# Kernel tuning notes

Measured on AMD Instinct MI355X. Metric: run time of the kernel, lower is better.

## Reference

```python
import jax, jax.numpy as jnp
import numpy as np

DIM = 768
HEADS = 8
DHEAD = 64
DEMB = HEADS * DHEAD  # 512
EPS = 1e-5


def layer_norm(x, g, b):
    mu = jnp.mean(x, axis=-1, keepdims=True)
    var = jnp.var(x, axis=-1, keepdims=True)
    return (x - mu) * jax.lax.rsqrt(var + EPS) * g + b


def setup_inputs() -> dict:
    key = jax.random.key(0)
    ks = jax.random.split(key, 9)
    b, t, n_src, n_ltn = 2, 4, 8192, 64
    inv = 1.0 / np.sqrt(DIM)
    return {
        "src": jax.random.normal(ks[0], (b, t, n_src, DIM), jnp.float32),
        "ltn": jax.random.normal(ks[1], (b, t, n_ltn, DIM), jnp.float32),
        "g_src": jnp.ones((DIM,), jnp.float32),
        "b_src": jnp.zeros((DIM,), jnp.float32),
        "g_ltn": jnp.ones((DIM,), jnp.float32),
        "b_ltn": jnp.zeros((DIM,), jnp.float32),
        # weights stored (in, out) so y = x @ W  (== torch Linear with W.T)
        "Wq": jax.random.normal(ks[2], (DIM, DEMB), jnp.float32) * inv,
        "Wkv": jax.random.normal(ks[3], (DIM, 2 * DEMB), jnp.float32) * inv,
        "Wo": jax.random.normal(ks[4], (DEMB, DIM), jnp.float32) * (1.0 / np.sqrt(DEMB)),
    }


def reference(src, ltn, g_src, b_src, g_ltn, b_ltn, Wq, Wkv, Wo):
    b, t, n_ltn, _ = ltn.shape
    n_src = src.shape[2]
    scale = DHEAD ** -0.5

    src_n = layer_norm(src, g_src, b_src)
    ltn_n = layer_norm(ltn, g_ltn, b_ltn)

    q = ltn_n @ Wq                                  # [b,t,nl,DEMB]
    ctx = jnp.concatenate([src_n, ltn_n], axis=-2)  # [b,t,ns+nl,DIM]
    kv = ctx @ Wkv                                  # [b,t,ns+nl,2*DEMB]
    k, v = jnp.split(kv, 2, axis=-1)

    def to_heads(x):  # b t n (h d) -> b h t n d
        B, T, N, _ = x.shape
        return x.reshape(B, T, N, HEADS, DHEAD).transpose(0, 3, 1, 2, 4)

    q, k, v = to_heads(q), to_heads(k), to_heads(v)

    attn = jnp.einsum('bhtid,bhtjd->bhtij', q, k) * scale
    attn = jax.nn.softmax(attn - jax.lax.stop_gradient(attn.max(axis=-1, keepdims=True)), axis=-1)
    out = jnp.einsum('bhtij,bhtjd->bhtid', attn, v)  # [b,h,t,nl,d]

    out = out.transpose(0, 2, 3, 1, 4).reshape(b, t, n_ltn, DEMB)
    return out @ Wo
```

## Files before the change

kernel.cpp:

```cpp
#include <hip/hip_runtime.h>
#include <hip/hip_bf16.h>
#include <type_traits>


#define N_SRC 8192
#define N_LTN 64
#define N_CTX 8256
#define NBT 8
#define MROWS 66048
#define DIMK 768
#define DEMB 512
#define NSPLIT 32
#define NTILES 65

typedef short short8 __attribute__((ext_vector_type(8)));
typedef float floatx4 __attribute__((ext_vector_type(4)));
typedef __attribute__((address_space(1))) void gvoid;
typedef __attribute__((address_space(3))) void lvoid;

__device__ inline ushort f2bf(float f) {
    union { float f; unsigned u; } v; v.f = f;
    unsigned u = v.u;
    return (ushort)((u + 0x7fffu + ((u >> 16) & 1u)) >> 16);
}

__global__ __launch_bounds__(256) void transpose_all(
        const float* __restrict__ Wkv, const float* __restrict__ Wq,
        const float* __restrict__ Wo, ushort* __restrict__ WkvT,
        ushort* __restrict__ WqT, ushort* __restrict__ WoT) {
    __shared__ ushort tile[64][65];
    int z = blockIdx.z;
    const float* in; ushort* out; int R, C;
    if (z == 0)      { in = Wkv; out = WkvT; R = 768; C = 1024; }
    else if (z == 1) { in = Wq;  out = WqT;  R = 768; C = 512;  }
    else             { in = Wo;  out = WoT;  R = 512; C = 768;  }
    int C0 = blockIdx.x * 64, R0 = blockIdx.y * 64;
    if (C0 >= C || R0 >= R) return;
    int tc = threadIdx.x & 63, tr4 = threadIdx.x >> 6;
#pragma unroll
    for (int j = 0; j < 16; j++) {
        int r = tr4 + j * 4;
        tile[r][tc] = f2bf(in[(size_t)(R0 + r) * C + C0 + tc]);
    }
    __syncthreads();
#pragma unroll
    for (int j = 0; j < 16; j++) {
        int c = tr4 + j * 4;
        out[(size_t)(C0 + c) * R + R0 + tc] = tile[tc][c];
    }
}

__global__ __launch_bounds__(256) void ln_kernel(
        const float* __restrict__ src, const float* __restrict__ ltn,
        const float* __restrict__ gs, const float* __restrict__ bs,
        const float* __restrict__ gl, const float* __restrict__ bl,
        ushort* __restrict__ ctx, ushort* __restrict__ qin) {
    int r = blockIdx.x * 4 + (threadIdx.x >> 6);
    int lane = threadIdx.x & 63;
    int bt = r / N_CTX;
    int i = r - bt * N_CTX;
    const float *x, *g, *b;
    int isl = (i >= N_SRC);
    if (!isl) { x = src + ((size_t)bt * N_SRC + i) * DIMK; g = gs; b = bs; }
    else      { x = ltn + ((size_t)bt * N_LTN + (i - N_SRC)) * DIMK; g = gl; b = bl; }
    float4 v[3]; float s = 0.f, s2 = 0.f;
#pragma unroll
    for (int t = 0; t < 3; t++) {
        float4 xv = *(const float4*)(x + t * 256 + lane * 4);
        v[t] = xv;
        s  += xv.x + xv.y + xv.z + xv.w;
        s2 += xv.x * xv.x + xv.y * xv.y + xv.z * xv.z + xv.w * xv.w;
    }
#pragma unroll
    for (int off = 32; off >= 1; off >>= 1) {
        s  += __shfl_xor(s,  off, 64);
        s2 += __shfl_xor(s2, off, 64);
    }
    float mu  = s * (1.0f / 768.0f);
    float var = s2 * (1.0f / 768.0f) - mu * mu;
    float rs  = rsqrtf(var + 1e-5f);
    ushort* crow = ctx + (size_t)r * DIMK;
    ushort* qrow = isl ? (qin + (size_t)(bt * N_LTN + (i - N_SRC)) * DIMK) : nullptr;
#pragma unroll
    for (int t = 0; t < 3; t++) {
        int idx = t * 256 + lane * 4;
        float4 gv = *(const float4*)(g + idx);
        float4 bv = *(const float4*)(b + idx);
        ushort4 u;
        u.x = f2bf((v[t].x - mu) * rs * gv.x + bv.x);
        u.y = f2bf((v[t].y - mu) * rs * gv.y + bv.y);
        u.z = f2bf((v[t].z - mu) * rs * gv.z + bv.z);
        u.w = f2bf((v[t].w - mu) * rs * gv.w + bv.w);
        *(ushort4*)(crow + idx) = u;
        if (isl) *(ushort4*)(qrow + idx) = u;
    }
}

template <typename CT>
__global__ __launch_bounds__(256) void gemm_bt(
        const ushort* __restrict__ A, const ushort* __restrict__ B,
        CT* __restrict__ C, int M, int N, int K) {
    __shared__ ushort lA[128 * 64];
    __shared__ ushort lB[128 * 64];
    int tid = threadIdx.x;
    int lane = tid & 63, wave = tid >> 6;
    int wm = wave >> 1, wn = wave & 1;
    int bn = blockIdx.x, bm = blockIdx.y;

    floatx4 acc[4][4];
#pragma unroll
    for (int mi = 0; mi < 4; mi++)
#pragma unroll
        for (int ni = 0; ni < 4; ni++) acc[mi][ni] = (floatx4){0.f, 0.f, 0.f, 0.f};

    int srow = lane >> 3;
    int schunk = (lane & 7) ^ srow;
    int quad = lane >> 4, lr = lane & 15;
    const int kiters = K >> 6;

    for (int kt = 0; kt < kiters; kt++) {
#pragma unroll
        for (int c2 = 0; c2 < 4; c2++) {
            int row = c2 * 32 + wave * 8 + srow;
            const ushort* gpA = A + ((size_t)(bm * 128 + row) * K + kt * 64 + schunk * 8);
            ushort* lpA = lA + (c2 * 32 + wave * 8) * 64 + lane * 8;
            __builtin_amdgcn_global_load_lds((gvoid*)gpA, (lvoid*)lpA, 16, 0, 0);
            const ushort* gpB = B + ((size_t)(bn * 128 + row) * K + kt * 64 + schunk * 8);
            ushort* lpB = lB + (c2 * 32 + wave * 8) * 64 + lane * 8;
            __builtin_amdgcn_global_load_lds((gvoid*)gpB, (lvoid*)lpB, 16, 0, 0);
        }
        __syncthreads();
#pragma unroll
        for (int ks = 0; ks < 2; ks++) {
            short8 av[4], bv[4];
            int slot = ((ks * 4 + quad) ^ (lane & 7)) * 8;
#pragma unroll
            for (int mi = 0; mi < 4; mi++)
                av[mi] = *(const short8*)(lA + (wm * 64 + mi * 16 + lr) * 64 + slot);
#pragma unroll
            for (int ni = 0; ni < 4; ni++)
                bv[ni] = *(const short8*)(lB + (wn * 64 + ni * 16 + lr) * 64 + slot);
#pragma unroll
            for (int mi = 0; mi < 4; mi++)
#pragma unroll
                for (int ni = 0; ni < 4; ni++)
                    acc[mi][ni] = __builtin_amdgcn_mfma_f32_16x16x32_bf16(
                        av[mi], bv[ni], acc[mi][ni], 0, 0, 0);
        }
        __syncthreads();
    }
#pragma unroll
    for (int mi = 0; mi < 4; mi++)
#pragma unroll
        for (int ni = 0; ni < 4; ni++)
#pragma unroll
            for (int r = 0; r < 4; r++) {
                int row = bm * 128 + wm * 64 + mi * 16 + quad * 4 + r;
                int col = bn * 128 + wn * 64 + ni * 16 + lr;
                float vv = acc[mi][ni][r];
                if constexpr (std::is_same<CT, ushort>::value)
                    C[(size_t)row * N + col] = f2bf(vv);
                else
                    C[(size_t)row * N + col] = vv;
            }
}

#define PR 136

__global__ __launch_bounds__(256) void attn_flash(
        const float* __restrict__ qf, const ushort* __restrict__ kvb,
        float* __restrict__ Op, float* __restrict__ ml) {
    __shared__ ushort lK[128 * 64];
    __shared__ ushort lVT[64 * PR];
    __shared__ ushort lP[64 * PR];
    __shared__ float smax[64 * 4];
    __shared__ float psum[64 * 4];
    __shared__ float mnew[64];
    __shared__ float salpha[64];

    int comb = blockIdx.x, split = blockIdx.y;
    int bt = comb >> 3, h = comb & 7;
    int tid = threadIdx.x;
    int w = tid >> 6, lane = tid & 63, quad = lane >> 4, lr = lane & 15;

    const ushort* kptr = kvb + (size_t)bt * N_CTX * 1024 + h * 64;
    const ushort* vptr = kptr + 512;

    short8 qa[4][2];
    {
        const float* qbase = qf + (size_t)(bt * 64) * DEMB + h * 64;
#pragma unroll
        for (int mi = 0; mi < 4; mi++)
#pragma unroll
            for (int kc = 0; kc < 2; kc++) {
                const float* p = qbase + (size_t)(mi * 16 + lr) * DEMB + kc * 32 + quad * 8;
                float4 f0 = *(const float4*)p;
                float4 f1 = *(const float4*)(p + 4);
                short8 v;
                v[0] = f2bf(f0.x); v[1] = f2bf(f0.y); v[2] = f2bf(f0.z); v[3] = f2bf(f0.w);
                v[4] = f2bf(f1.x); v[5] = f2bf(f1.y); v[6] = f2bf(f1.z); v[7] = f2bf(f1.w);
                qa[mi][kc] = v;
            }
    }

    floatx4 accO[4];
#pragma unroll
    for (int nt = 0; nt < 4; nt++) accO[nt] = (floatx4){0.f, 0.f, 0.f, 0.f};
    float m_run = -1e30f, l_run = 0.f;

    int vp = tid & 63;
    int vdg = tid >> 6;

    for (int t = split; t < NTILES; t += NSPLIT) {
        int kbase = t * 128;
        __syncthreads();

#pragma unroll
        for (int c2 = 0; c2 < 4; c2++) {
            int jloc = w * 32 + c2 * 8 + (lane >> 3);
            int chunk = (lane & 7) ^ ((lane >> 3) & 7);
            int jg = kbase + jloc; if (jg > N_CTX - 1) jg = N_CTX - 1;
            const ushort* gp = kptr + (size_t)jg * 1024 + chunk * 8;
            ushort* lp = lK + (w * 32 + c2 * 8) * 64 + lane * 8;
            __builtin_amdgcn_global_load_lds((gvoid*)gp, (lvoid*)lp, 16, 0, 0);
        }

        {
            int k0 = kbase + vp * 2;
            bool valid = (k0 + 1) < N_CTX;
            int k0c = valid ? k0 : (N_CTX - 2);
            const ushort* r0 = vptr + (size_t)k0c * 1024 + vdg * 16;
            const ushort* r1 = r0 + 1024;
            uint4 a0 = *(const uint4*)r0;
            uint4 a1 = *(const uint4*)(r0 + 8);
            uint4 b0 = *(const uint4*)r1;
            uint4 b1 = *(const uint4*)(r1 + 8);
            if (!valid) {
                a0 = make_uint4(0, 0, 0, 0); a1 = a0; b0 = a0; b1 = a0;
            }
            unsigned av8[8] = {a0.x, a0.y, a0.z, a0.w, a1.x, a1.y, a1.z, a1.w};
            unsigned bv8[8] = {b0.x, b0.y, b0.z, b0.w, b1.x, b1.y, b1.z, b1.w};
#pragma unroll
            for (int i = 0; i < 8; i++) {
                unsigned la = av8[i] & 0xffffu, ha = av8[i] >> 16;
                unsigned lb = bv8[i] & 0xffffu, hb = bv8[i] >> 16;
                *(unsigned*)(lVT + (vdg * 16 + 2 * i) * PR + vp * 2)     = la | (lb << 16);
                *(unsigned*)(lVT + (vdg * 16 + 2 * i + 1) * PR + vp * 2) = ha | (hb << 16);
            }
        }
        __syncthreads();

        floatx4 accS[4][2];
#pragma unroll
        for (int mi = 0; mi < 4; mi++)
#pragma unroll
            for (int nt = 0; nt < 2; nt++) accS[mi][nt] = (floatx4){0.f, 0.f, 0.f, 0.f};
#pragma unroll
        for (int kc = 0; kc < 2; kc++) {
            short8 bv[2];
#pragma unroll
            for (int nt = 0; nt < 2; nt++) {
                int kr = w * 32 + nt * 16 + lr;
                int slot = (kc * 4 + quad) ^ (kr & 7);
                bv[nt] = *(const short8*)(lK + kr * 64 + slot * 8);
            }
#pragma unroll
            for (int mi = 0; mi < 4; mi++)
#pragma unroll
                for (int nt = 0; nt < 2; nt++)
                    accS[mi][nt] = __builtin_amdgcn_mfma_f32_16x16x32_bf16(
                        qa[mi][kc], bv[nt], accS[mi][nt], 0, 0, 0);
        }

        bool v0 = (kbase + w * 32 + lr) < N_CTX;
        bool v1 = (kbase + w * 32 + 16 + lr) < N_CTX;
        float sc[4][2][4];
#pragma unroll
        for (int mi = 0; mi < 4; mi++)
#pragma unroll
            for (int r = 0; r < 4; r++) {
                sc[mi][0][r] = v0 ? accS[mi][0][r] * 0.125f : -1e30f;
                sc[mi][1][r] = v1 ? accS[mi][1][r] * 0.125f : -1e30f;
            }
#pragma unroll
        for (int mi = 0; mi < 4; mi++)
#pragma unroll
            for (int r = 0; r < 4; r++) {
                float m = fmaxf(sc[mi][0][r], sc[mi][1][r]);
#pragma unroll
                for (int d = 1; d < 16; d <<= 1) m = fmaxf(m, __shfl_xor(m, d, 64));
                if (lr == 0) smax[(mi * 16 + quad * 4 + r) * 4 + w] = m;
            }
        __syncthreads();

        if (w == 0) {
            float4 s4 = *(const float4*)(smax + lane * 4);
            float mt = fmaxf(fmaxf(s4.x, s4.y), fmaxf(s4.z, s4.w));
            float mn = fmaxf(m_run, mt);
            salpha[lane] = __expf(m_run - mn);
            m_run = mn;
            mnew[lane] = mn;
        }
        __syncthreads();

#pragma unroll
        for (int mi = 0; mi < 4; mi++)
#pragma unroll
            for (int r = 0; r < 4; r++) {
                int row = mi * 16 + quad * 4 + r;
                float mrow = mnew[row];
                float p0 = __expf(sc[mi][0][r] - mrow);
                float p1 = __expf(sc[mi][1][r] - mrow);
                lP[row * PR + w * 32 + lr]      = f2bf(p0);
                lP[row * PR + w * 32 + 16 + lr] = f2bf(p1);
                float s = p0 + p1;
#pragma unroll
                for (int d = 1; d < 16; d <<= 1) s += __shfl_xor(s, d, 64);
                if (lr == 0) psum[row * 4 + w] = s;
            }
        {
            float a0 = salpha[w * 16 + quad * 4 + 0];
            float a1 = salpha[w * 16 + quad * 4 + 1];
            float a2 = salpha[w * 16 + quad * 4 + 2];
            float a3 = salpha[w * 16 + quad * 4 + 3];
#pragma unroll
            for (int nt = 0; nt < 4; nt++) {
                accO[nt][0] *= a0; accO[nt][1] *= a1;
                accO[nt][2] *= a2; accO[nt][3] *= a3;
            }
        }
        __syncthreads();

        if (w == 0) {
            float4 p4 = *(const float4*)(psum + lane * 4);
            l_run = l_run * salpha[lane] + (p4.x + p4.y + p4.z + p4.w);
        }

        short8 av[4];
#pragma unroll
        for (int kc = 0; kc < 4; kc++)
            av[kc] = *(const short8*)(lP + (w * 16 + lr) * PR + kc * 32 + quad * 8);
#pragma unroll
        for (int nt = 0; nt < 4; nt++)
#pragma unroll
            for (int kc = 0; kc < 4; kc++) {
                short8 bv = *(const short8*)(lVT + (nt * 16 + lr) * PR + kc * 32 + quad * 8);
                accO[nt] = __builtin_amdgcn_mfma_f32_16x16x32_bf16(av[kc], bv, accO[nt], 0, 0, 0);
            }
    }

    float* opb = Op + (size_t)(comb * NSPLIT + split) * 64 * 64;
#pragma unroll
    for (int nt = 0; nt < 4; nt++)
#pragma unroll
        for (int r = 0; r < 4; r++)
            opb[(w * 16 + quad * 4 + r) * 64 + nt * 16 + lr] = accO[nt][r];
    if (w == 0) {
        float* mlp = ml + ((size_t)(comb * NSPLIT + split) * 64 + lane) * 2;
        mlp[0] = m_run; mlp[1] = l_run;
    }
}

__global__ __launch_bounds__(64) void attn_combine(
        const float* __restrict__ Op, const float* __restrict__ ml,
        ushort* __restrict__ outp) {
    int bx = blockIdx.x;
    int comb = bx >> 6, q = bx & 63;
    int bt = comb >> 3, h = comb & 7;
    int d = threadIdx.x;
    float M = -1e30f;
    for (int s = 0; s < NSPLIT; s++)
        M = fmaxf(M, ml[((size_t)(comb * NSPLIT + s) * 64 + q) * 2]);
    float L = 0.f, O = 0.f;
    for (int s = 0; s < NSPLIT; s++) {
        const float* p = ml + ((size_t)(comb * NSPLIT + s) * 64 + q) * 2;
        float wgt = __expf(p[0] - M);
        L = fmaf(wgt, p[1], L);
        O = fmaf(wgt, Op[((size_t)(comb * NSPLIT + s) * 64 + q) * 64 + d], O);
    }
    outp[(size_t)(bt * 64 + q) * DEMB + h * 64 + d] = f2bf(O / L);
}

extern "C" void kernel_launch(void* const* d_in, const int* in_sizes, int n_in,
                              void* d_out, int out_size, void* d_ws, size_t ws_size,
                              hipStream_t stream) {
    const float* src   = (const float*)d_in[0];
    const float* ltn   = (const float*)d_in[1];
    const float* g_src = (const float*)d_in[2];
    const float* b_src = (const float*)d_in[3];
    const float* g_ltn = (const float*)d_in[4];
    const float* b_ltn = (const float*)d_in[5];
    const float* Wq    = (const float*)d_in[6];
    const float* Wkv   = (const float*)d_in[7];
    const float* Wo    = (const float*)d_in[8];
    float* out = (float*)d_out;

    char* ws = (char*)d_ws;
    size_t off = 0;
    auto alloc = [&](size_t bytes) -> void* {
        void* p = ws + off;
        off += (bytes + 255) & ~(size_t)255;
        return p;
    };
    ushort* ctx  = (ushort*)alloc((size_t)MROWS * DIMK * 2);
    ushort* qin  = (ushort*)alloc((size_t)512 * DIMK * 2);
    ushort* WkvT = (ushort*)alloc((size_t)1024 * DIMK * 2);
    ushort* WqT  = (ushort*)alloc((size_t)512 * DIMK * 2);
    ushort* WoT  = (ushort*)alloc((size_t)768 * DEMB * 2);
    ushort* kvb  = (ushort*)alloc((size_t)MROWS * 1024 * 2);
    float*  qf   = (float*) alloc((size_t)512 * DEMB * 4);
    ushort* outp = (ushort*)alloc((size_t)512 * DEMB * 2);

    float* Op  = (float*)(void*)ctx;
    float* mlb = Op + (size_t)64 * NSPLIT * 64 * 64;

    transpose_all<<<dim3(16, 12, 3), 256, 0, stream>>>(Wkv, Wq, Wo, WkvT, WqT, WoT);

    ln_kernel<<<MROWS / 4, 256, 0, stream>>>(src, ltn, g_src, b_src, g_ltn, b_ltn, ctx, qin);

    gemm_bt<ushort><<<dim3(1024 / 128, MROWS / 128), 256, 0, stream>>>(
        ctx, WkvT, kvb, MROWS, 1024, DIMK);
    gemm_bt<float><<<dim3(512 / 128, 512 / 128), 256, 0, stream>>>(
        qin, WqT, qf, 512, 512, DIMK);

    attn_flash<<<dim3(64, NSPLIT), 256, 0, stream>>>(qf, kvb, Op, mlb);
    attn_combine<<<4096, 64, 0, stream>>>(Op, mlb, outp);

    gemm_bt<float><<<dim3(768 / 128, 512 / 128), 256, 0, stream>>>(
        outp, WoT, out, 512, 768, DEMB);
}
```

Baseline: 568.5 us.

## Give each wave its own query rows in flash attention and halve the split count

Restructures the attention kernel so that each wave owns 16 query rows across all 128 keys of a tile, not 32 keys across all 64 rows. Row max and row sum now come from in-wave shuffles, which removes the shared-memory reduction arrays and two block barriers per tile. The number of KV splits drops from 32 to 16, so each block handles more tiles, the grid shrinks, and the combine step reads fewer partials. In exchange, each wave holds more score registers and reads all 128 K rows from LDS, and the smaller grid may leave compute units underused.

```diff
diff --git a/kernel.cpp b/kernel.cpp
--- a/kernel.cpp
+++ b/kernel.cpp
@@ -10,7 +10,7 @@
 #define MROWS 66048
 #define DIMK 768
 #define DEMB 512
-#define NSPLIT 32
+#define NSPLIT 16
 #define NTILES 65
 
 typedef short short8 __attribute__((ext_vector_type(8)));
@@ -173,10 +173,6 @@
     __shared__ ushort lK[128 * 64];
     __shared__ ushort lVT[64 * PR];
     __shared__ ushort lP[64 * PR];
-    __shared__ float smax[64 * 4];
-    __shared__ float psum[64 * 4];
-    __shared__ float mnew[64];
-    __shared__ float salpha[64];
 
     int comb = blockIdx.x, split = blockIdx.y;
     int bt = comb >> 3, h = comb & 7;
@@ -186,30 +182,27 @@
     const ushort* kptr = kvb + (size_t)bt * N_CTX * 1024 + h * 64;
     const ushort* vptr = kptr + 512;
 
-    short8 qa[4][2];
+    short8 qa[2];
     {
-        const float* qbase = qf + (size_t)(bt * 64) * DEMB + h * 64;
-#pragma unroll
-        for (int mi = 0; mi < 4; mi++)
-#pragma unroll
-            for (int kc = 0; kc < 2; kc++) {
-                const float* p = qbase + (size_t)(mi * 16 + lr) * DEMB + kc * 32 + quad * 8;
-                float4 f0 = *(const float4*)p;
-                float4 f1 = *(const float4*)(p + 4);
-                short8 v;
-                v[0] = f2bf(f0.x); v[1] = f2bf(f0.y); v[2] = f2bf(f0.z); v[3] = f2bf(f0.w);
-                v[4] = f2bf(f1.x); v[5] = f2bf(f1.y); v[6] = f2bf(f1.z); v[7] = f2bf(f1.w);
-                qa[mi][kc] = v;
-            }
+        const float* p0 = qf + (size_t)(bt * 64 + w * 16 + lr) * DEMB + h * 64;
+#pragma unroll
+        for (int kc = 0; kc < 2; kc++) {
+            const float* p = p0 + kc * 32 + quad * 8;
+            float4 f0 = *(const float4*)p;
+            float4 f1 = *(const float4*)(p + 4);
+            short8 v;
+            v[0] = f2bf(f0.x); v[1] = f2bf(f0.y); v[2] = f2bf(f0.z); v[3] = f2bf(f0.w);
+            v[4] = f2bf(f1.x); v[5] = f2bf(f1.y); v[6] = f2bf(f1.z); v[7] = f2bf(f1.w);
+            qa[kc] = v;
+        }
     }
 
     floatx4 accO[4];
 #pragma unroll
     for (int nt = 0; nt < 4; nt++) accO[nt] = (floatx4){0.f, 0.f, 0.f, 0.f};
-    float m_run = -1e30f, l_run = 0.f;
-
-    int vp = tid & 63;
-    int vdg = tid >> 6;
+    float m_run[4], l_run[4];
+#pragma unroll
+    for (int r = 0; r < 4; r++) { m_run[r] = -1e30f; l_run[r] = 0.f; }
 
     for (int t = split; t < NTILES; t += NSPLIT) {
         int kbase = t * 128;
@@ -226,10 +219,10 @@
         }
 
         {
-            int k0 = kbase + vp * 2;
+            int k0 = kbase + lane * 2;
             bool valid = (k0 + 1) < N_CTX;
             int k0c = valid ? k0 : (N_CTX - 2);
-            const ushort* r0 = vptr + (size_t)k0c * 1024 + vdg * 16;
+            const ushort* r0 = vptr + (size_t)k0c * 1024 + w * 16;
             const ushort* r1 = r0 + 1024;
             uint4 a0 = *(const uint4*)r0;
             uint4 a1 = *(const uint4*)(r0 + 8);
@@ -244,96 +237,72 @@
             for (int i = 0; i < 8; i++) {
                 unsigned la = av8[i] & 0xffffu, ha = av8[i] >> 16;
                 unsigned lb = bv8[i] & 0xffffu, hb = bv8[i] >> 16;
-                *(unsigned*)(lVT + (vdg * 16 + 2 * i) * PR + vp * 2)     = la | (lb << 16);
-                *(unsigned*)(lVT + (vdg * 16 + 2 * i + 1) * PR + vp * 2) = ha | (hb << 16);
+                *(unsigned*)(lVT + (w * 16 + 2 * i) * PR + lane * 2)     = la | (lb << 16);
+                *(unsigned*)(lVT + (w * 16 + 2 * i + 1) * PR + lane * 2) = ha | (hb << 16);
             }
         }
         __syncthreads();
 
-        floatx4 accS[4][2];
-#pragma unroll
-        for (int mi = 0; mi < 4; mi++)
-#pragma unroll
-            for (int nt = 0; nt < 2; nt++) accS[mi][nt] = (floatx4){0.f, 0.f, 0.f, 0.f};
+        floatx4 accS[8];
+#pragma unroll
+        for (int nt = 0; nt < 8; nt++) accS[nt] = (floatx4){0.f, 0.f, 0.f, 0.f};
 #pragma unroll
         for (int kc = 0; kc < 2; kc++) {
-            short8 bv[2];
-#pragma unroll
-            for (int nt = 0; nt < 2; nt++) {
-                int kr = w * 32 + nt * 16 + lr;
+#pragma unroll
+            for (int nt = 0; nt < 8; nt++) {
+                int kr = nt * 16 + lr;
                 int slot = (kc * 4 + quad) ^ (kr & 7);
-                bv[nt] = *(const short8*)(lK + kr * 64 + slot * 8);
-            }
-#pragma unroll
-            for (int mi = 0; mi < 4; mi++)
-#pragma unroll
-                for (int nt = 0; nt < 2; nt++)
-                    accS[mi][nt] = __builtin_amdgcn_mfma_f32_16x16x32_bf16(
-                        qa[mi][kc], bv[nt], accS[mi][nt], 0, 0, 0);
-        }
-
-        bool v0 = (kbase + w * 32 + lr) < N_CTX;
-        bool v1 = (kbase + w * 32 + 16 + lr) < N_CTX;
-        float sc[4][2][4];
-#pragma unroll
-        for (int mi = 0; mi < 4; mi++)
+                short8 bv = *(const short8*)(lK + kr * 64 + slot * 8);
+                accS[nt] = __builtin_amdgcn_mfma_f32_16x16x32_bf16(
+                    qa[kc], bv, accS[nt], 0, 0, 0);
+            }
+        }
+
+        float sc[8][4];
+        float tmax[4] = {-1e30f, -1e30f, -1e30f, -1e30f};
+#pragma unroll
+        for (int nt = 0; nt < 8; nt++) {
+            bool vk = (kbase + nt * 16 + lr) < N_CTX;
 #pragma unroll
             for (int r = 0; r < 4; r++) {
-                sc[mi][0][r] = v0 ? accS[mi][0][r] * 0.125f : -1e30f;
-                sc[mi][1][r] = v1 ? accS[mi][1][r] * 0.125f : -1e30f;
-            }
-#pragma unroll
-        for (int mi = 0; mi < 4; mi++)
+                float s = vk ? accS[nt][r] * 0.125f : -1e30f;
+                sc[nt][r] = s;
+                tmax[r] = fmaxf(tmax[r], s);
+            }
+        }
+#pragma unroll
+        for (int r = 0; r < 4; r++) {
+#pragma unroll
+            for (int d = 1; d < 16; d <<= 1) tmax[r] = fmaxf(tmax[r], __shfl_xor(tmax[r], d, 64));
+        }
+        float alpha[4], lsum[4];
+#pragma unroll
+        for (int r = 0; r < 4; r++) {
+            float mn = fmaxf(m_run[r], tmax[r]);
+            alpha[r] = __expf(m_run[r] - mn);
+            m_run[r] = mn;
+            lsum[r] = 0.f;
+        }
+
+#pragma unroll
+        for (int nt = 0; nt < 8; nt++) {
 #pragma unroll
             for (int r = 0; r < 4; r++) {
-                float m = fmaxf(sc[mi][0][r], sc[mi][1][r]);
-#pragma unroll
-                for (int d = 1; d < 16; d <<= 1) m = fmaxf(m, __shfl_xor(m, d, 64));
-                if (lr == 0) smax[(mi * 16 + quad * 4 + r) * 4 + w] = m;
-            }
-        __syncthreads();
-
-        if (w == 0) {
-            float4 s4 = *(const float4*)(smax + lane * 4);
-            float mt = fmaxf(fmaxf(s4.x, s4.y), fmaxf(s4.z, s4.w));
-            float mn = fmaxf(m_run, mt);
-            salpha[lane] = __expf(m_run - mn);
-            m_run = mn;
-            mnew[lane] = mn;
-        }
-        __syncthreads();
-
-#pragma unroll
-        for (int mi = 0; mi < 4; mi++)
-#pragma unroll
-            for (int r = 0; r < 4; r++) {
-                int row = mi * 16 + quad * 4 + r;
-                float mrow = mnew[row];
-                float p0 = __expf(sc[mi][0][r] - mrow);
-                float p1 = __expf(sc[mi][1][r] - mrow);
-                lP[row * PR + w * 32 + lr]      = f2bf(p0);
-                lP[row * PR + w * 32 + 16 + lr] = f2bf(p1);
-                float s = p0 + p1;
-#pragma unroll
-                for (int d = 1; d < 16; d <<= 1) s += __shfl_xor(s, d, 64);
-                if (lr == 0) psum[row * 4 + w] = s;
-            }
-        {
-            float a0 = salpha[w * 16 + quad * 4 + 0];
-            float a1 = salpha[w * 16 + quad * 4 + 1];
-            float a2 = salpha[w * 16 + quad * 4 + 2];
-            float a3 = salpha[w * 16 + quad * 4 + 3];
-#pragma unroll
-            for (int nt = 0; nt < 4; nt++) {
-                accO[nt][0] *= a0; accO[nt][1] *= a1;
-                accO[nt][2] *= a2; accO[nt][3] *= a3;
-            }
-        }
-        __syncthreads();
-
-        if (w == 0) {
-            float4 p4 = *(const float4*)(psum + lane * 4);
-            l_run = l_run * salpha[lane] + (p4.x + p4.y + p4.z + p4.w);
+                float p = __expf(sc[nt][r] - m_run[r]);
+                lsum[r] += p;
+                lP[(w * 16 + quad * 4 + r) * PR + nt * 16 + lr] = f2bf(p);
+            }
+        }
+#pragma unroll
+        for (int r = 0; r < 4; r++) {
+#pragma unroll
+            for (int d = 1; d < 16; d <<= 1) lsum[r] += __shfl_xor(lsum[r], d, 64);
+            l_run[r] = l_run[r] * alpha[r] + lsum[r];
+        }
+#pragma unroll
+        for (int nt = 0; nt < 4; nt++) {
+            accO[nt][0] *= alpha[0]; accO[nt][1] *= alpha[1];
+            accO[nt][2] *= alpha[2]; accO[nt][3] *= alpha[3];
         }
 
         short8 av[4];
@@ -355,9 +324,13 @@
 #pragma unroll
         for (int r = 0; r < 4; r++)
             opb[(w * 16 + quad * 4 + r) * 64 + nt * 16 + lr] = accO[nt][r];
-    if (w == 0) {
-        float* mlp = ml + ((size_t)(comb * NSPLIT + split) * 64 + lane) * 2;
-        mlp[0] = m_run; mlp[1] = l_run;
+    if (lr == 0) {
+#pragma unroll
+        for (int r = 0; r < 4; r++) {
+            int row = w * 16 + quad * 4 + r;
+            float* mlp = ml + ((size_t)(comb * NSPLIT + split) * 64 + row) * 2;
+            mlp[0] = m_run[r]; mlp[1] = l_run[r];
+        }
     }
 }
 
```

Result: faster. 531.2 us (-6.6%).
